# Kernel optimization log

Hardware: AMD Instinct MI355X
Metric: run time of the kernel (lower is better)

The kernel has to match this reference:

```python
import jax, jax.numpy as jnp
import numpy as np


def _bitrev_indices(N):
    # bit-reversal permutation, vectorized in numpy (static, N known at trace time)
    bits = int(np.log2(N))
    idx = np.arange(N, dtype=np.int64)
    rev = np.zeros(N, dtype=np.int64)
    for _ in range(bits):
        rev = (rev << 1) | (idx & 1)
        idx >>= 1
    return jnp.asarray(rev)


def setup_inputs() -> dict:
    key = jax.random.key(0)
    k1, k2 = jax.random.split(key)
    B, N = 2048, 4096
    return {
        "x_re": jax.random.normal(k1, (B, N), dtype=jnp.float32),
        "x_im": jax.random.normal(k2, (B, N), dtype=jnp.float32),
    }


def reference(x_re, x_im):
    # Radix-2 decimation-in-time Cooley-Tukey FFT, faithful to PythonFFT.forward
    N = x_re.shape[-1]
    batch = x_re.shape[:-1]
    num_stages = int(np.log2(N))

    # twiddle table W_N^k = exp(-2*pi*i*k/N) (matches compute_twiddle_table)
    k = jnp.arange(N, dtype=jnp.float32)
    angles = (-2.0 * np.pi) * k / N
    W_re_tab = jnp.cos(angles)
    W_im_tab = jnp.sin(angles)

    br = _bitrev_indices(N)
    y_re = x_re[..., br]
    y_im = x_im[..., br]

    # loop over log2(N) stages (small fixed loop); each stage is fully vectorized
    for stage in range(num_stages):
        stride = 1 << stage
        group = stride << 1
        # twiddle index for butterfly position j in a group: j * (N // group) % N
        tw_idx = (jnp.arange(stride) * (N // group)) % N
        w_re = W_re_tab[tw_idx]  # [stride]
        w_im = W_im_tab[tw_idx]  # [stride]

        yr = y_re.reshape(*batch, N // group, 2, stride)
        yi = y_im.reshape(*batch, N // group, 2, stride)
        a_re, b_re = yr[..., 0, :], yr[..., 1, :]
        a_im, b_im = yi[..., 0, :], yi[..., 1, :]

        wb_re = w_re * b_re - w_im * b_im
        wb_im = w_re * b_im + w_im * b_re

        y_re = jnp.stack([a_re + wb_re, a_re - wb_re], axis=-2).reshape(*batch, N)
        y_im = jnp.stack([a_im + wb_im, a_im - wb_im], axis=-2).reshape(*batch, N)

    return (y_re, y_im)
```

## Files before the change

kernel.cpp:

```cpp
#include <hip/hip_runtime.h>
#include <math.h>

#define FFT_N   4096
#define THREADS 256
#define RH 0.70710678118654752f
#define C16 0.92387953251128676f
#define S16 0.38268343236508977f
#define NEG2PI_256  (-2.45436926061702597e-2f)
#define NEG2PI_4096 (-1.53398078788564123e-3f)

#define POS(k) ((((k) & 3) << 2) | ((k) >> 2))

__device__ __forceinline__ float2 cmul(float2 a, float2 b) {
    return make_float2(a.x * b.x - a.y * b.y, a.x * b.y + a.y * b.x);
}

__device__ __forceinline__ void bar_lds() {
    asm volatile("s_waitcnt lgkmcnt(0)" ::: "memory");
    __builtin_amdgcn_s_barrier();
}

__device__ __forceinline__ void dft4(float2& a, float2& b, float2& c, float2& d) {
    float2 t0 = make_float2(a.x + c.x, a.y + c.y);
    float2 t1 = make_float2(a.x - c.x, a.y - c.y);
    float2 t2 = make_float2(b.x + d.x, b.y + d.y);
    float2 t3 = make_float2(b.y - d.y, d.x - b.x);
    a = make_float2(t0.x + t2.x, t0.y + t2.y);
    b = make_float2(t1.x + t3.x, t1.y + t3.y);
    c = make_float2(t0.x - t2.x, t0.y - t2.y);
    d = make_float2(t1.x - t3.x, t1.y - t3.y);
}

template<int E>
__device__ __forceinline__ float2 mw16(float2 z) {
    if constexpr (E == 0) return z;
    else if constexpr (E == 4) return make_float2(z.y, -z.x);
    else if constexpr (E == 2) return make_float2(RH * (z.x + z.y), RH * (z.y - z.x));
    else if constexpr (E == 6) return make_float2(RH * (z.y - z.x), -RH * (z.x + z.y));
    else if constexpr (E == 1) return cmul(z, make_float2(C16, -S16));
    else if constexpr (E == 3) return cmul(z, make_float2(S16, -C16));
    else           return cmul(z, make_float2(-C16, S16));
}

__device__ __forceinline__ void dft16(float2 (&v)[16]) {
    dft4(v[0], v[4], v[8],  v[12]);
    dft4(v[1], v[5], v[9],  v[13]);
    dft4(v[2], v[6], v[10], v[14]);
    dft4(v[3], v[7], v[11], v[15]);
    v[5]  = mw16<1>(v[5]);   v[9]  = mw16<2>(v[9]);   v[13] = mw16<3>(v[13]);
    v[6]  = mw16<2>(v[6]);   v[10] = mw16<4>(v[10]);  v[14] = mw16<6>(v[14]);
    v[7]  = mw16<3>(v[7]);   v[11] = mw16<6>(v[11]);  v[15] = mw16<9>(v[15]);
    dft4(v[0],  v[1],  v[2],  v[3]);
    dft4(v[4],  v[5],  v[6],  v[7]);
    dft4(v[8],  v[9],  v[10], v[11]);
    dft4(v[12], v[13], v[14], v[15]);
}

__device__ __forceinline__ void load_row(float2 (&v)[16],
                                         const float* __restrict__ xr,
                                         const float* __restrict__ xi, int t) {
    #pragma unroll
    for (int n3 = 0; n3 < 16; ++n3) {
        v[n3].x = xr[t + (n3 << 8)];
        v[n3].y = xi[t + (n3 << 8)];
    }
}

__device__ __forceinline__ void process_row(float2 (&v)[16], float2* __restrict__ sd,
                                            int t, int lo, int hi,
                                            float* __restrict__ yr,
                                            float* __restrict__ yi) {
    dft16(v);

    {
        float sn, cs;
        __sincosf((float)hi * NEG2PI_256, &sn, &cs);
        float2 b[4], c[4];
        b[0] = make_float2(1.f, 0.f);
        b[1] = make_float2(cs, sn);
        b[2] = cmul(b[1], b[1]);
        b[3] = cmul(b[2], b[1]);
        c[0] = make_float2(1.f, 0.f);
        c[1] = cmul(b[2], b[2]);
        c[2] = cmul(c[1], c[1]);
        c[3] = cmul(c[2], c[1]);
        #pragma unroll
        for (int k3 = 0; k3 < 16; ++k3) {
            float2 z = v[POS(k3)];
            if (k3 & 3)  z = cmul(z, b[k3 & 3]);
            if (k3 >> 2) z = cmul(z, c[k3 >> 2]);
            sd[t + (k3 << 8)] = z;
        }
    }
    bar_lds();

    #pragma unroll
    for (int n2 = 0; n2 < 16; ++n2)
        v[n2] = sd[lo + (n2 << 4) + (hi << 8)];
    bar_lds();

    dft16(v);

    {
        float sn, cs;
        __sincosf((float)(lo * hi) * NEG2PI_4096, &sn, &cs);
        const float2 P = make_float2(cs, sn);
        __sincosf((float)lo * NEG2PI_256, &sn, &cs);
        float2 w1 = make_float2(cs, sn);
        float2 w2 = cmul(w1, w1);
        float2 w3 = cmul(w2, w1);
        float2 Pw[4], z[4];
        Pw[0] = P;
        Pw[1] = cmul(P, w1);
        Pw[2] = cmul(P, w2);
        Pw[3] = cmul(P, w3);
        z[0] = make_float2(1.f, 0.f);
        z[1] = cmul(w2, w2);
        z[2] = cmul(z[1], z[1]);
        z[3] = cmul(z[2], z[1]);
        const int wb = (hi ^ lo) + (lo << 8);
        #pragma unroll
        for (int k2 = 0; k2 < 16; ++k2) {
            float2 u = cmul(v[POS(k2)], Pw[k2 & 3]);
            if (k2 >> 2) u = cmul(u, z[k2 >> 2]);
            sd[wb + (k2 << 4)] = u;
        }
    }
    bar_lds();

    #pragma unroll
    for (int m = 0; m < 16; ++m)
        v[m] = sd[(lo ^ m) + (hi << 4) + (m << 8)];

    dft16(v);
    #pragma unroll
    for (int k1 = 0; k1 < 16; ++k1) {
        __builtin_nontemporal_store(v[POS(k1)].x, &yr[t + (k1 << 8)]);
        __builtin_nontemporal_store(v[POS(k1)].y, &yi[t + (k1 << 8)]);
    }
}

__global__ __launch_bounds__(THREADS)
void fft4096_r16p(const float* __restrict__ xre, const float* __restrict__ xim,
                  float* __restrict__ yre, float* __restrict__ yim)
{
    __shared__ float2 sd[FFT_N];

    const int t  = threadIdx.x;
    const int lo = t & 15;
    const int hi = t >> 4;
    const size_t off0 = (size_t)(2 * blockIdx.x) * FFT_N;
    const size_t off1 = off0 + FFT_N;

    float2 va[16], vb[16];
    load_row(va, xre + off0, xim + off0, t);
    load_row(vb, xre + off1, xim + off1, t);

    process_row(va, sd, t, lo, hi, yre + off0, yim + off0);
    bar_lds();
    process_row(vb, sd, t, lo, hi, yre + off1, yim + off1);
}

extern "C" void kernel_launch(void* const* d_in, const int* in_sizes, int n_in,
                              void* d_out, int out_size, void* d_ws, size_t ws_size,
                              hipStream_t stream) {
    const float* xre = (const float*)d_in[0];
    const float* xim = (const float*)d_in[1];
    const int total = in_sizes[0];
    const int rows  = total / FFT_N;
    float* yre = (float*)d_out;
    float* yim = yre + total;
    fft4096_r16p<<<dim3(rows / 2), dim3(THREADS), 0, stream>>>(xre, xim, yre, yim);
}
```

Before: 26.47 us.

## Process four rows per block with software-pipelined prefetch and hoisted twiddles

Each block now handles four FFT rows instead of two. The next row's global loads are issued in the middle of the current row's processing, so they overlap with its LDS passes. The per-thread twiddle factors are computed once per block rather than once per row, and the barrier is emitted as one asm block. In exchange the grid halves to 512 blocks, which reduces parallelism across CUs, and holding the prefetched row raises register pressure.

```diff
diff --git a/kernel.cpp b/kernel.cpp
--- a/kernel.cpp
+++ b/kernel.cpp
@@ -3,6 +3,7 @@
 
 #define FFT_N   4096
 #define THREADS 256
+#define RPB     4
 #define RH 0.70710678118654752f
 #define C16 0.92387953251128676f
 #define S16 0.38268343236508977f
@@ -16,8 +17,7 @@
 }
 
 __device__ __forceinline__ void bar_lds() {
-    asm volatile("s_waitcnt lgkmcnt(0)" ::: "memory");
-    __builtin_amdgcn_s_barrier();
+    asm volatile("s_waitcnt lgkmcnt(0)\n\ts_barrier" ::: "memory");
 }
 
 __device__ __forceinline__ void dft4(float2& a, float2& b, float2& c, float2& d) {
@@ -56,41 +56,23 @@
     dft4(v[12], v[13], v[14], v[15]);
 }
 
-__device__ __forceinline__ void load_row(float2 (&v)[16],
-                                         const float* __restrict__ xr,
-                                         const float* __restrict__ xi, int t) {
-    #pragma unroll
-    for (int n3 = 0; n3 < 16; ++n3) {
-        v[n3].x = xr[t + (n3 << 8)];
-        v[n3].y = xi[t + (n3 << 8)];
-    }
-}
-
-__device__ __forceinline__ void process_row(float2 (&v)[16], float2* __restrict__ sd,
-                                            int t, int lo, int hi,
-                                            float* __restrict__ yr,
-                                            float* __restrict__ yi) {
+template<bool PF>
+__device__ __forceinline__ void process_row(
+    float2 (&v)[16], float2 (&vn)[16], float2* __restrict__ sd,
+    const int t, const int lo, const int hi,
+    const float2 (&b)[4], const float2 (&c)[4],
+    const float2 (&Pw)[4], const float2 (&zz)[4], const int wb2,
+    const float* __restrict__ xr_n, const float* __restrict__ xi_n,
+    float* __restrict__ yr, float* __restrict__ yi)
+{
     dft16(v);
 
-    {
-        float sn, cs;
-        __sincosf((float)hi * NEG2PI_256, &sn, &cs);
-        float2 b[4], c[4];
-        b[0] = make_float2(1.f, 0.f);
-        b[1] = make_float2(cs, sn);
-        b[2] = cmul(b[1], b[1]);
-        b[3] = cmul(b[2], b[1]);
-        c[0] = make_float2(1.f, 0.f);
-        c[1] = cmul(b[2], b[2]);
-        c[2] = cmul(c[1], c[1]);
-        c[3] = cmul(c[2], c[1]);
-        #pragma unroll
-        for (int k3 = 0; k3 < 16; ++k3) {
-            float2 z = v[POS(k3)];
-            if (k3 & 3)  z = cmul(z, b[k3 & 3]);
-            if (k3 >> 2) z = cmul(z, c[k3 >> 2]);
-            sd[t + (k3 << 8)] = z;
-        }
+    #pragma unroll
+    for (int k3 = 0; k3 < 16; ++k3) {
+        float2 z = v[POS(k3)];
+        if (k3 & 3)  z = cmul(z, b[k3 & 3]);
+        if (k3 >> 2) z = cmul(z, c[k3 >> 2]);
+        sd[t + (k3 << 8)] = z;
     }
     bar_lds();
 
@@ -101,29 +83,18 @@
 
     dft16(v);
 
-    {
-        float sn, cs;
-        __sincosf((float)(lo * hi) * NEG2PI_4096, &sn, &cs);
-        const float2 P = make_float2(cs, sn);
-        __sincosf((float)lo * NEG2PI_256, &sn, &cs);
-        float2 w1 = make_float2(cs, sn);
-        float2 w2 = cmul(w1, w1);
-        float2 w3 = cmul(w2, w1);
-        float2 Pw[4], z[4];
-        Pw[0] = P;
-        Pw[1] = cmul(P, w1);
-        Pw[2] = cmul(P, w2);
-        Pw[3] = cmul(P, w3);
-        z[0] = make_float2(1.f, 0.f);
-        z[1] = cmul(w2, w2);
-        z[2] = cmul(z[1], z[1]);
-        z[3] = cmul(z[2], z[1]);
-        const int wb = (hi ^ lo) + (lo << 8);
+    #pragma unroll
+    for (int k2 = 0; k2 < 16; ++k2) {
+        float2 u = cmul(v[POS(k2)], Pw[k2 & 3]);
+        if (k2 >> 2) u = cmul(u, zz[k2 >> 2]);
+        sd[wb2 + (k2 << 4)] = u;
+    }
+
+    if constexpr (PF) {
         #pragma unroll
-        for (int k2 = 0; k2 < 16; ++k2) {
-            float2 u = cmul(v[POS(k2)], Pw[k2 & 3]);
-            if (k2 >> 2) u = cmul(u, z[k2 >> 2]);
-            sd[wb + (k2 << 4)] = u;
+        for (int n3 = 0; n3 < 16; ++n3) {
+            vn[n3].x = xr_n[t + (n3 << 8)];
+            vn[n3].y = xi_n[t + (n3 << 8)];
         }
     }
     bar_lds();
@@ -138,10 +109,11 @@
         __builtin_nontemporal_store(v[POS(k1)].x, &yr[t + (k1 << 8)]);
         __builtin_nontemporal_store(v[POS(k1)].y, &yi[t + (k1 << 8)]);
     }
+    bar_lds();
 }
 
 __global__ __launch_bounds__(THREADS)
-void fft4096_r16p(const float* __restrict__ xre, const float* __restrict__ xim,
+void fft4096_pipe(const float* __restrict__ xre, const float* __restrict__ xim,
                   float* __restrict__ yre, float* __restrict__ yim)
 {
     __shared__ float2 sd[FFT_N];
@@ -149,16 +121,57 @@
     const int t  = threadIdx.x;
     const int lo = t & 15;
     const int hi = t >> 4;
-    const size_t off0 = (size_t)(2 * blockIdx.x) * FFT_N;
-    const size_t off1 = off0 + FFT_N;
+
+    float2 b[4], c[4], Pw[4], zz[4];
+    {
+        float sn, cs;
+        __sincosf((float)hi * NEG2PI_256, &sn, &cs);
+        b[0] = make_float2(1.f, 0.f);
+        b[1] = make_float2(cs, sn);
+        b[2] = cmul(b[1], b[1]);
+        b[3] = cmul(b[2], b[1]);
+        c[0] = make_float2(1.f, 0.f);
+        c[1] = cmul(b[2], b[2]);
+        c[2] = cmul(c[1], c[1]);
+        c[3] = cmul(c[2], c[1]);
+        __sincosf((float)(lo * hi) * NEG2PI_4096, &sn, &cs);
+        const float2 P = make_float2(cs, sn);
+        __sincosf((float)lo * NEG2PI_256, &sn, &cs);
+        float2 w1 = make_float2(cs, sn);
+        float2 w2 = cmul(w1, w1);
+        float2 w3 = cmul(w2, w1);
+        Pw[0] = P;
+        Pw[1] = cmul(P, w1);
+        Pw[2] = cmul(P, w2);
+        Pw[3] = cmul(P, w3);
+        zz[0] = make_float2(1.f, 0.f);
+        zz[1] = cmul(w2, w2);
+        zz[2] = cmul(zz[1], zz[1]);
+        zz[3] = cmul(zz[2], zz[1]);
+    }
+    const int wb2 = (lo ^ hi) + (lo << 8);
+
+    const size_t r0 = (size_t)blockIdx.x * RPB * FFT_N;
+    const float* xr = xre + r0;
+    const float* xi = xim + r0;
+    float*       yr = yre + r0;
+    float*       yi = yim + r0;
 
     float2 va[16], vb[16];
-    load_row(va, xre + off0, xim + off0, t);
-    load_row(vb, xre + off1, xim + off1, t);
+    #pragma unroll
+    for (int n3 = 0; n3 < 16; ++n3) {
+        va[n3].x = xr[t + (n3 << 8)];
+        va[n3].y = xi[t + (n3 << 8)];
+    }
 
-    process_row(va, sd, t, lo, hi, yre + off0, yim + off0);
-    bar_lds();
-    process_row(vb, sd, t, lo, hi, yre + off1, yim + off1);
+    process_row<true >(va, vb, sd, t, lo, hi, b, c, Pw, zz, wb2,
+                       xr + FFT_N,     xi + FFT_N,     yr,             yi);
+    process_row<true >(vb, va, sd, t, lo, hi, b, c, Pw, zz, wb2,
+                       xr + 2 * FFT_N, xi + 2 * FFT_N, yr + FFT_N,     yi + FFT_N);
+    process_row<true >(va, vb, sd, t, lo, hi, b, c, Pw, zz, wb2,
+                       xr + 3 * FFT_N, xi + 3 * FFT_N, yr + 2 * FFT_N, yi + 2 * FFT_N);
+    process_row<false>(vb, va, sd, t, lo, hi, b, c, Pw, zz, wb2,
+                       xr,             xi,             yr + 3 * FFT_N, yi + 3 * FFT_N);
 }
 
 extern "C" void kernel_launch(void* const* d_in, const int* in_sizes, int n_in,
@@ -170,5 +183,5 @@
     const int rows  = total / FFT_N;
     float* yre = (float*)d_out;
     float* yim = yre + total;
-    fft4096_r16p<<<dim3(rows / 2), dim3(THREADS), 0, stream>>>(xre, xim, yre, yim);
+    fft4096_pipe<<<dim3(rows / RPB), dim3(THREADS), 0, stream>>>(xre, xim, yre, yim);
 }
```

After: 26.85 us. Within noise of the previous version (+1.4%).
